# Performance work log

Hardware: AMD Instinct MI355X
Metric: run time of the kernel (lower is better)

## Reference

```python
import jax, jax.numpy as jnp
import numpy as np


def _min_dist(src, tgt):
    # Euclidean cdist via the |a|^2 + |b|^2 - 2ab expansion (same math as torch.cdist p=2),
    # then row-wise min/argmin. src: (S,3), tgt: (T,3) -> (S,), (S,)
    d2 = (
        jnp.sum(src * src, axis=1)[:, None]
        + jnp.sum(tgt * tgt, axis=1)[None, :]
        - 2.0 * (src @ tgt.T)
    )
    d = jnp.sqrt(jnp.maximum(d2, 0.0))
    return jnp.min(d, axis=1), jnp.argmin(d, axis=1)


def setup_inputs() -> dict:
    key = jax.random.key(0)
    k1, k2, k3 = jax.random.split(key, 3)
    N, M = 32768, 8192
    P = jax.random.normal(k1, (N, 3), dtype=jnp.float32)
    Ps = jax.random.normal(k2, (M, 3), dtype=jnp.float32)
    probabilities = jax.random.uniform(k3, (M,), dtype=jnp.float32)
    return {"P": P, "Ps": Ps, "probabilities": probabilities}


def reference(P, Ps, probabilities):
    # sampled -> original: min distance per sampled point
    dist_s_to_o, _ = _min_dist(Ps, P)
    # original -> sampled: min distance + index of nearest sampled point
    dist_o_to_s, min_indices = _min_dist(P, Ps)
    weighted_s_to_o = dist_s_to_o * probabilities
    weighted_o_to_s = dist_o_to_s * probabilities[min_indices]
    return weighted_s_to_o.sum() + weighted_o_to_s.sum()
```

## Files before the change

### kernel.cpp

```cpp
#include <hip/hip_runtime.h>
#include <math.h>

static constexpr int BLK = 256;
static constexpr int CH = 2048;
static constexpr int SUB = 256;
static constexpr int QB = 128;

typedef _Float16 f16x8 __attribute__((ext_vector_type(8)));
typedef float f32x16 __attribute__((ext_vector_type(16)));

__device__ __forceinline__ unsigned f2u(float f) { return __float_as_uint(f); }
__device__ __forceinline__ float u2f(unsigned u) { return __uint_as_float(u); }
__device__ __forceinline__ unsigned pk(_Float16 a, _Float16 b) {
    union { _Float16 h[2]; unsigned u; } c; c.h[0] = a; c.h[1] = b; return c.u;
}
union B128 { uint4 u; f16x8 h; };

__global__ void prep_kernel(unsigned long long* __restrict__ o2s,
                            unsigned* __restrict__ s2o,
                            float* __restrict__ out, int N, int M) {
    int i = blockIdx.x * blockDim.x + threadIdx.x;
    if (i < N) o2s[i] = ~0ull;
    if (i < M) s2o[i] = 0xFFFFFFFFu;
    if (i == 0) out[0] = 0.0f;
}

__global__ void __launch_bounds__(BLK)
__attribute__((amdgpu_waves_per_eu(4, 4))) main_kernel(
    const float* __restrict__ P, const float* __restrict__ Ps,
    unsigned long long* __restrict__ o2s, unsigned* __restrict__ s2o,
    int N, int M, int o2sBlocks, int o2sRG, int s2oRG) {
    __shared__ uint4 lds16[SUB + 1];
    int tid = threadIdx.x;
    int lane = tid & 63, wave = tid >> 6;
    int n = lane & 31, half = lane >> 5;
    if (tid == 0) lds16[SUB] = make_uint4(0u, 0u, 0u, 0u);

    int bx = blockIdx.x;
    bool isO2S = bx < o2sBlocks;
    const float* qsrc; const float* ssrc;
    int i0, j0, scnt;
    if (isO2S) {
        int rg = bx % o2sRG, c = bx / o2sRG;
        i0 = rg * QB + wave * 32; j0 = c * CH; scnt = M;
        qsrc = P; ssrc = Ps;
    } else {
        int b = bx - o2sBlocks;
        int rg = b % s2oRG, c = b / s2oRG;
        i0 = rg * QB + wave * 32; j0 = c * CH; scnt = N;
        qsrc = Ps; ssrc = P;
    }

    f16x8 af;
    {
        float x = 0.f, y = 0.f, z = 0.f;
        if (half == 0) {
            int i = i0 + n;
            x = qsrc[3 * i]; y = qsrc[3 * i + 1]; z = qsrc[3 * i + 2];
        }
        _Float16 hx = (_Float16)x, hy = (_Float16)y, hz = (_Float16)z;
        _Float16 one = (half == 0) ? (_Float16)1.0f : (_Float16)0.0f;
        af = (f16x8){(_Float16)-hx, (_Float16)-hy, (_Float16)-hz, one,
                     (_Float16)0.0f, (_Float16)0.0f, (_Float16)0.0f, (_Float16)0.0f};
    }

    float runm[16];
#pragma unroll
    for (int r = 0; r < 16; ++r) runm[r] = __builtin_inff();
    f32x16 zacc = {};

    for (int s = 0; s < CH / SUB; ++s) {
        __syncthreads();
        {
            int jj = j0 + s * SUB + tid;
            jj = min(jj, scnt - 1);
            float x = ssrc[3 * jj], y = ssrc[3 * jj + 1], z = ssrc[3 * jj + 2];
            _Float16 hx = (_Float16)x, hy = (_Float16)y, hz = (_Float16)z;
            float fx = (float)hx, fy = (float)hy, fz = (float)hz;
            _Float16 hw = (_Float16)(0.5f * (fx * fx + fy * fy + fz * fz));
            lds16[tid] = make_uint4(pk(hx, hy), pk(hz, hw), 0u, 0u);
        }
        __syncthreads();
#pragma unroll
        for (int t = 0; t < SUB / 32; t += 2) {
            B128 bva, bvb;
            bva.u = lds16[half ? SUB : (t * 32 + n)];
            bvb.u = lds16[half ? SUB : ((t + 1) * 32 + n)];
            f32x16 ca = __builtin_amdgcn_mfma_f32_32x32x16_f16(af, bva.h, zacc, 0, 0, 0);
            f32x16 cb = __builtin_amdgcn_mfma_f32_32x32x16_f16(af, bvb.h, zacc, 0, 0, 0);
            unsigned tga = (unsigned)(s * 8 + t), tgb = (unsigned)(s * 8 + t + 1);
            if (isO2S) {
#pragma unroll
                for (int r = 0; r < 16; ++r) {
                    float pa = u2f((f2u(ca[r]) & ~63u) | tga);
                    float pb = u2f((f2u(cb[r]) & ~63u) | tgb);
                    runm[r] = fminf(fminf(runm[r], pa), pb);
                }
            } else {
#pragma unroll
                for (int r = 0; r < 16; ++r)
                    runm[r] = fminf(fminf(runm[r], ca[r]), cb[r]);
            }
        }
    }

    if (isO2S) {
#pragma unroll
        for (int r = 0; r < 16; ++r) {
            unsigned u = f2u(runm[r]);
            unsigned full = ((u & 63u) << 5) | (unsigned)n;
            runm[r] = u2f((u & ~0x7FFu) | full);
        }
    }
#pragma unroll
    for (int mask = 1; mask < 32; mask <<= 1) {
#pragma unroll
        for (int r = 0; r < 16; ++r)
            runm[r] = fminf(runm[r], __shfl_xor(runm[r], mask, 64));
    }
    if (n < 16) {
        int r = n;
        int row = (r & 3) + 8 * (r >> 2) + 4 * half;
        int i = i0 + row;
        float x = qsrc[3 * i], y = qsrc[3 * i + 1], z = qsrc[3 * i + 2];
        _Float16 hx = (_Float16)x, hy = (_Float16)y, hz = (_Float16)z;
        float fx = (float)hx, fy = (float)hy, fz = (float)hz;
        float pw = 0.5f * (fx * fx + fy * fy + fz * fz);
        float v = runm[r];
        float d2 = fmaxf(2.0f * (pw + v), 0.0f);
        if (isO2S) {
            unsigned jloc = f2u(v) & 0x7FFu;
            unsigned long long key =
                ((unsigned long long)f2u(d2) << 32) | (unsigned)(j0 + (int)jloc);
            atomicMin(&o2s[i], key);
        } else {
            atomicMin(&s2o[i], f2u(d2));
        }
    }
}

__global__ void finish_kernel(const unsigned* __restrict__ s2o,
                              const unsigned long long* __restrict__ o2s,
                              const float* __restrict__ prob,
                              float* __restrict__ out, int N, int M) {
    int t = blockIdx.x * BLK + threadIdx.x;
    float acc = 0.0f;
    if (t < M) {
        acc = sqrtf(u2f(s2o[t])) * prob[t];
    } else if (t < M + N) {
        unsigned long long key = o2s[t - M];
        float d2 = u2f((unsigned)(key >> 32));
        unsigned jj = (unsigned)(key & 0xFFFFFFFFu);
        acc = sqrtf(d2) * prob[jj];
    }
#pragma unroll
    for (int off = 32; off > 0; off >>= 1) acc += __shfl_down(acc, off, 64);
    __shared__ float wsum[BLK / 64];
    int lane = threadIdx.x & 63, wave = threadIdx.x >> 6;
    if (lane == 0) wsum[wave] = acc;
    __syncthreads();
    if (threadIdx.x == 0) {
        float s = 0.0f;
#pragma unroll
        for (int w = 0; w < BLK / 64; ++w) s += wsum[w];
        atomicAdd(out, s);
    }
}

extern "C" void kernel_launch(void* const* d_in, const int* in_sizes, int n_in,
                              void* d_out, int out_size, void* d_ws, size_t ws_size,
                              hipStream_t stream) {
    const float* P = (const float*)d_in[0];
    const float* Ps = (const float*)d_in[1];
    const float* prob = (const float*)d_in[2];
    int N = in_sizes[0] / 3;
    int M = in_sizes[1] / 3;
    float* out = (float*)d_out;

    unsigned long long* o2s = (unsigned long long*)d_ws;
    unsigned* s2o = (unsigned*)((char*)d_ws + (size_t)N * 8);

    int o2sRG = N / QB;
    int s2oRG = M / QB;
    int o2sBlocks = o2sRG * (M / CH);
    int s2oBlocks = s2oRG * (N / CH);
    int total = o2sBlocks + s2oBlocks;

    prep_kernel<<<(N + BLK - 1) / BLK, BLK, 0, stream>>>(o2s, s2o, out, N, M);
    main_kernel<<<total, BLK, 0, stream>>>(P, Ps, o2s, s2o, N, M,
                                           o2sBlocks, o2sRG, s2oRG);
    finish_kernel<<<(N + M + BLK - 1) / BLK, BLK, 0, stream>>>(s2o, o2s, prob,
                                                               out, N, M);
}
```

Measured before the change: 96.83 us.

## Track per-subchunk min without index tagging and recover argmin by rescanning candidates

The inner loop no longer tags each MFMA result with a tile index. It takes a plain min over four MFMA tiles into a per-subchunk accumulator and tags only once per 256-point subchunk with the subchunk id. The epilogue then recomputes the 8 candidate distances in that subchunk's column in fp32 to recover the exact argmin index. This removes the per-element bitmask/or ALU work from the hot loop, at the cost of extra global loads and arithmetic in the epilogue. Masking the low 8 bits of the float instead of 6 slightly reduces comparison precision.

```diff
diff --git a/kernel.cpp b/kernel.cpp
--- a/kernel.cpp
+++ b/kernel.cpp
@@ -81,26 +81,34 @@
             lds16[tid] = make_uint4(pk(hx, hy), pk(hz, hw), 0u, 0u);
         }
         __syncthreads();
-#pragma unroll
-        for (int t = 0; t < SUB / 32; t += 2) {
-            B128 bva, bvb;
-            bva.u = lds16[half ? SUB : (t * 32 + n)];
-            bvb.u = lds16[half ? SUB : ((t + 1) * 32 + n)];
-            f32x16 ca = __builtin_amdgcn_mfma_f32_32x32x16_f16(af, bva.h, zacc, 0, 0, 0);
-            f32x16 cb = __builtin_amdgcn_mfma_f32_32x32x16_f16(af, bvb.h, zacc, 0, 0, 0);
-            unsigned tga = (unsigned)(s * 8 + t), tgb = (unsigned)(s * 8 + t + 1);
-            if (isO2S) {
-#pragma unroll
-                for (int r = 0; r < 16; ++r) {
-                    float pa = u2f((f2u(ca[r]) & ~63u) | tga);
-                    float pb = u2f((f2u(cb[r]) & ~63u) | tgb);
-                    runm[r] = fminf(fminf(runm[r], pa), pb);
-                }
-            } else {
-#pragma unroll
-                for (int r = 0; r < 16; ++r)
-                    runm[r] = fminf(fminf(runm[r], ca[r]), cb[r]);
+        float smin[16];
+#pragma unroll
+        for (int r = 0; r < 16; ++r) smin[r] = __builtin_inff();
+#pragma unroll
+        for (int t = 0; t < SUB / 32; t += 4) {
+            B128 b0, b1, b2, b3;
+            b0.u = lds16[half ? SUB : ((t + 0) * 32 + n)];
+            b1.u = lds16[half ? SUB : ((t + 1) * 32 + n)];
+            b2.u = lds16[half ? SUB : ((t + 2) * 32 + n)];
+            b3.u = lds16[half ? SUB : ((t + 3) * 32 + n)];
+            f32x16 c0 = __builtin_amdgcn_mfma_f32_32x32x16_f16(af, b0.h, zacc, 0, 0, 0);
+            f32x16 c1 = __builtin_amdgcn_mfma_f32_32x32x16_f16(af, b1.h, zacc, 0, 0, 0);
+            f32x16 c2 = __builtin_amdgcn_mfma_f32_32x32x16_f16(af, b2.h, zacc, 0, 0, 0);
+            f32x16 c3 = __builtin_amdgcn_mfma_f32_32x32x16_f16(af, b3.h, zacc, 0, 0, 0);
+#pragma unroll
+            for (int r = 0; r < 16; ++r) {
+                smin[r] = fminf(fminf(smin[r], c0[r]), c1[r]);
+                smin[r] = fminf(fminf(smin[r], c2[r]), c3[r]);
             }
+        }
+        if (isO2S) {
+#pragma unroll
+            for (int r = 0; r < 16; ++r)
+                runm[r] = fminf(runm[r], u2f((f2u(smin[r]) & ~0xFFu) | (unsigned)s));
+        } else {
+#pragma unroll
+            for (int r = 0; r < 16; ++r)
+                runm[r] = fminf(runm[r], smin[r]);
         }
     }
 
@@ -108,8 +116,7 @@
 #pragma unroll
         for (int r = 0; r < 16; ++r) {
             unsigned u = f2u(runm[r]);
-            unsigned full = ((u & 63u) << 5) | (unsigned)n;
-            runm[r] = u2f((u & ~0x7FFu) | full);
+            runm[r] = u2f((u & ~0xFFu) | ((u & 7u) << 5) | (unsigned)n);
         }
     }
 #pragma unroll
@@ -125,15 +132,30 @@
         float x = qsrc[3 * i], y = qsrc[3 * i + 1], z = qsrc[3 * i + 2];
         _Float16 hx = (_Float16)x, hy = (_Float16)y, hz = (_Float16)z;
         float fx = (float)hx, fy = (float)hy, fz = (float)hz;
+        float nx = -fx, ny = -fy, nz = -fz;
         float pw = 0.5f * (fx * fx + fy * fy + fz * fz);
-        float v = runm[r];
-        float d2 = fmaxf(2.0f * (pw + v), 0.0f);
         if (isO2S) {
-            unsigned jloc = f2u(v) & 0x7FFu;
+            unsigned uv = f2u(runm[r]);
+            int sWin = (int)((uv >> 5) & 7u);
+            int col = (int)(uv & 31u);
+            float best = __builtin_inff();
+            int bj = 0;
+#pragma unroll
+            for (int t = 0; t < 8; ++t) {
+                int j = j0 + sWin * SUB + t * 32 + col;
+                float sx = (float)(_Float16)ssrc[3 * j];
+                float sy = (float)(_Float16)ssrc[3 * j + 1];
+                float sz = (float)(_Float16)ssrc[3 * j + 2];
+                float sw = 0.5f * (sx * sx + sy * sy + sz * sz);
+                float m = fmaf(sx, nx, fmaf(sy, ny, fmaf(sz, nz, sw)));
+                if (m < best) { best = m; bj = j; }
+            }
+            float d2 = fmaxf(2.0f * (pw + best), 0.0f);
             unsigned long long key =
-                ((unsigned long long)f2u(d2) << 32) | (unsigned)(j0 + (int)jloc);
+                ((unsigned long long)f2u(d2) << 32) | (unsigned)bj;
             atomicMin(&o2s[i], key);
         } else {
+            float d2 = fmaxf(2.0f * (pw + runm[r]), 0.0f);
             atomicMin(&s2o[i], f2u(d2));
         }
     }
```

New measurement: 91.76 us. -5.2%, faster.
